# Kernel tuning notes

Hardware: AMD Instinct MI355X
Metric: run time of the kernel (lower is better)

The kernel has to match this reference:

```python
import jax, jax.numpy as jnp
import numpy as np

NUM_EMB = 16384
EMB_DIM = 64
BETA = 0.25  # commitment_cost, legacy=True formulation


def _l2norm(x, axis=-1):
    # matches F.normalize(p=2): x / max(||x||, 1e-12)
    n = jnp.sqrt(jnp.sum(x * x, axis=axis, keepdims=True))
    return x / jnp.maximum(n, 1e-12)


def setup_inputs() -> dict:
    key = jax.random.key(0)
    k_z, k_cb, k_w, k_b = jax.random.split(key, 4)
    z = jax.random.normal(k_z, (16, 1024, EMB_DIM), dtype=jnp.float32)
    # frozen codebook: N(0, d^{-0.5})
    codebook = jax.random.normal(k_cb, (NUM_EMB, EMB_DIM), dtype=jnp.float32) * (EMB_DIM ** -0.5)
    # Linear(d, d) default init: U(-1/sqrt(d), 1/sqrt(d))
    lim = 1.0 / np.sqrt(EMB_DIM)
    proj_w = jax.random.uniform(k_w, (EMB_DIM, EMB_DIM), dtype=jnp.float32, minval=-lim, maxval=lim)
    proj_b = jax.random.uniform(k_b, (EMB_DIM,), dtype=jnp.float32, minval=-lim, maxval=lim)
    scale = jnp.float32(10.0)  # l2_norm_scale
    return {"z": z, "codebook": codebook, "proj_w": proj_w, "proj_b": proj_b, "scale": scale}


def reference(z, codebook, proj_w, proj_b, scale):
    B, T, d = z.shape
    zf = z.reshape(-1, d)                                   # [BT, d]
    quant_codebook = codebook @ proj_w.T + proj_b           # [N, d]
    zn = _l2norm(zf)
    cn = _l2norm(quant_codebook)
    distances = -jnp.einsum('bd,nd->bn', zn, cn) * scale    # [BT, N]
    idx = jnp.argmin(distances, axis=1)                     # [BT]
    quantized = quant_codebook[idx].reshape(z.shape)        # [B, T, d]
    sg = jax.lax.stop_gradient
    commitment_loss = jnp.mean((sg(quantized) - z) ** 2)
    codebook_loss = jnp.mean((quantized - sg(z)) ** 2)
    vq_loss = commitment_loss + BETA * codebook_loss        # legacy=True
    quantized_st = z + sg(quantized - z)                    # straight-through
    return quantized_st, vq_loss, idx.reshape(B, T)
```

## Files before the change

### kernel.cpp

```cpp
#include <hip/hip_runtime.h>
#include <hip/hip_bf16.h>


#define NCODES 16384
#define NTOK   16384
#define DIM    64
#define MARGIN_MFMA 8e-3f

typedef __attribute__((ext_vector_type(8))) short bf16x8;
typedef __attribute__((ext_vector_type(4))) float f32x4;
#define GLOBAL_AS __attribute__((address_space(1)))
#define LDS_AS    __attribute__((address_space(3)))

__device__ float  g_qcb[NCODES * DIM];
__device__ double g_cn64[NCODES * DIM];
__device__ short  g_cnb[NCODES * DIM];
__device__ short  g_znb[NTOK * DIM];
__device__ unsigned g_topu[NTOK];
__device__ int    g_candcnt[NTOK];
__device__ int    g_cand[NTOK * 8];
__device__ int    g_idx[NTOK];
__device__ int    g_ovcnt;
__device__ int    g_ovlist[NTOK];
__device__ float  g_loss;
__device__ int    g_done;

__device__ __forceinline__ float wave_sum64(float v) {
#pragma unroll
  for (int o = 32; o > 0; o >>= 1) v += __shfl_xor(v, o, 64);
  return v;
}
__device__ __forceinline__ double wave_sum64d(double v) {
#pragma unroll
  for (int o = 32; o > 0; o >>= 1) v += __shfl_xor(v, o, 64);
  return v;
}
__device__ __forceinline__ short f2bf(float f) {
  __hip_bfloat16 h = __float2bfloat16(f);
  return *reinterpret_cast<short*>(&h);
}

__global__ __launch_bounds__(256) void k_prep(const float* __restrict__ cb,
                                              const float* __restrict__ pw,
                                              const float* __restrict__ pb,
                                              const float* __restrict__ z) {
  int tid = threadIdx.x;
  if (blockIdx.x < 512) {
    __shared__ float Wt[64 * 65];
    __shared__ float cbs[32 * 65];
    int base = blockIdx.x * 32;
    for (int e = tid; e < 4096; e += 256) {
      int j = e >> 6, k = e & 63;
      Wt[k * 65 + j] = pw[e];
    }
    for (int e = tid; e < 2048; e += 256) {
      int row = e >> 6, k = e & 63;
      cbs[row * 65 + k] = cb[(size_t)(base + row) * 64 + k];
    }
    __syncthreads();
    int w = tid >> 6, j = tid & 63;
    double bj = (double)pb[j];
    for (int rr = 0; rr < 8; ++rr) {
      int nl = w * 8 + rr;
      int n = base + nl;
      double acc = bj;
#pragma unroll
      for (int k = 0; k < 64; ++k)
        acc = fma((double)cbs[nl * 65 + k], (double)Wt[k * 65 + j], acc);
      g_qcb[(size_t)n * 64 + j] = (float)acc;
      double tot = wave_sum64d(acc * acc);
      double cn = acc / fmax(sqrt(tot), 1e-12);
      g_cn64[(size_t)n * 64 + j] = cn;
      g_cnb[(size_t)n * 64 + j] = f2bf((float)cn);
    }
  } else {
    int zb = blockIdx.x - 512;
    int gid = zb * 256 + tid;
    if (gid < NTOK) { g_topu[gid] = 0u; g_candcnt[gid] = 0; }
    if (gid == 0) { g_loss = 0.f; g_ovcnt = 0; g_done = 0; }
    int w = tid >> 6, j = tid & 63;
    int base = zb * 64;
    for (int r = 0; r < 16; ++r) {
      int row = base + w * 16 + r;
      float v = z[(size_t)row * 64 + j];
      float tot = wave_sum64(v * v);
      g_znb[(size_t)row * 64 + j] = f2bf(v / fmaxf(sqrtf(tot), 1e-12f));
    }
  }
}


__global__ __launch_bounds__(256) void k_mfma1() {
  __shared__ __align__(16) short smB[2][8192];
  int tid = threadIdx.x;
  int wave = tid >> 6, lane = tid & 63;
  int quad = lane >> 4, col = lane & 15;
  int tokBlock = blockIdx.x >> 3, split = blockIdx.x & 7;
  int tokBase = tokBlock * 128 + wave * 32;

  const short* za = g_znb + (size_t)(tokBase + col) * 64 + quad * 8;
  bf16x8 A0[2], A1[2];
#pragma unroll
  for (int f = 0; f < 2; ++f) {
    A0[f] = *(const bf16x8*)(za + f * 16 * 64);
    A1[f] = *(const bf16x8*)(za + f * 16 * 64 + 32);
  }
  float m[2][4];
#pragma unroll
  for (int f = 0; f < 2; ++f)
#pragma unroll
    for (int r = 0; r < 4; ++r) m[f][r] = -3.0e38f;

  const char* gsplit = (const char*)(g_cnb + (size_t)split * 2048 * 64);
  int x = col & 7;
  int s0off = ((quad ^ x) << 3);
  int s1off = (((4 | quad) ^ x) << 3);

  int goff[4];
#pragma unroll
  for (int i = 0; i < 4; ++i) {
    int cidx = wave * 256 + i * 64 + lane;
    int row = cidx >> 3, sw = cidx & 7;
    goff[i] = row * 128 + (sw ^ (row & 7)) * 16;
  }

#pragma unroll
  for (int i = 0; i < 4; ++i)
    __builtin_amdgcn_global_load_lds((const GLOBAL_AS void*)(gsplit + goff[i]),
                                     (LDS_AS void*)(&smB[0][wave * 2048 + i * 512]), 16, 0, 0);
  __syncthreads();

  int p = 0;
  for (int s = 0; s < 16; ++s) {
    if (s < 15) {
      const char* gb = gsplit + (size_t)(s + 1) * 16384;
#pragma unroll
      for (int i = 0; i < 4; ++i)
        __builtin_amdgcn_global_load_lds((const GLOBAL_AS void*)(gb + goff[i]),
                                         (LDS_AS void*)(&smB[p ^ 1][wave * 2048 + i * 512]),
                                         16, 0, 0);
    }
    const short* bufp = smB[p];
#pragma unroll
    for (int t = 0; t < 8; ++t) {
      const short* lb = bufp + (t * 16 + col) * 64;
      bf16x8 b0 = *(const bf16x8*)(lb + s0off);
      bf16x8 b1 = *(const bf16x8*)(lb + s1off);
#pragma unroll
      for (int f = 0; f < 2; ++f) {
        f32x4 acc = {0.f, 0.f, 0.f, 0.f};
        acc = __builtin_amdgcn_mfma_f32_16x16x32_bf16(A0[f], b0, acc, 0, 0, 0);
        acc = __builtin_amdgcn_mfma_f32_16x16x32_bf16(A1[f], b1, acc, 0, 0, 0);
#pragma unroll
        for (int r = 0; r < 4; ++r) m[f][r] = fmaxf(m[f][r], acc[r]);
      }
    }
    __syncthreads();
    p ^= 1;
  }

#pragma unroll
  for (int f = 0; f < 2; ++f)
#pragma unroll
    for (int r = 0; r < 4; ++r) {
      float v = m[f][r];
      v = fmaxf(v, __shfl_xor(v, 1, 64));
      v = fmaxf(v, __shfl_xor(v, 2, 64));
      v = fmaxf(v, __shfl_xor(v, 4, 64));
      v = fmaxf(v, __shfl_xor(v, 8, 64));
      if (col == 0) {
        unsigned b = __float_as_uint(v);
        unsigned e = (b & 0x80000000u) ? ~b : (b | 0x80000000u);
        atomicMax(&g_topu[tokBase + f * 16 + quad * 4 + r], e);
      }
    }
}

__global__ __launch_bounds__(256) void k_mfma2() {
  __shared__ __align__(16) short smB[2][8192];
  int tid = threadIdx.x;
  int wave = tid >> 6, lane = tid & 63;
  int quad = lane >> 4, col = lane & 15;
  int tokBlock = blockIdx.x >> 3, split = blockIdx.x & 7;
  int tokBase = tokBlock * 128 + wave * 32;

  const short* za = g_znb + (size_t)(tokBase + col) * 64 + quad * 8;
  bf16x8 A0[2], A1[2];
#pragma unroll
  for (int f = 0; f < 2; ++f) {
    A0[f] = *(const bf16x8*)(za + f * 16 * 64);
    A1[f] = *(const bf16x8*)(za + f * 16 * 64 + 32);
  }
  float th[2][4];
#pragma unroll
  for (int f = 0; f < 2; ++f)
#pragma unroll
    for (int r = 0; r < 4; ++r) {
      unsigned u = g_topu[tokBase + f * 16 + quad * 4 + r];
      unsigned b = (u & 0x80000000u) ? (u & 0x7FFFFFFFu) : ~u;
      th[f][r] = __uint_as_float(b) - MARGIN_MFMA;
    }

  const char* gsplit = (const char*)(g_cnb + (size_t)split * 2048 * 64);
  int x = col & 7;
  int s0off = ((quad ^ x) << 3);
  int s1off = (((4 | quad) ^ x) << 3);

  int goff[4];
#pragma unroll
  for (int i = 0; i < 4; ++i) {
    int cidx = wave * 256 + i * 64 + lane;
    int row = cidx >> 3, sw = cidx & 7;
    goff[i] = row * 128 + (sw ^ (row & 7)) * 16;
  }

#pragma unroll
  for (int i = 0; i < 4; ++i)
    __builtin_amdgcn_global_load_lds((const GLOBAL_AS void*)(gsplit + goff[i]),
                                     (LDS_AS void*)(&smB[0][wave * 2048 + i * 512]), 16, 0, 0);
  __syncthreads();

  int codeB = split * 2048 + col;
  int p = 0;
  for (int s = 0; s < 16; ++s) {
    if (s < 15) {
      const char* gb = gsplit + (size_t)(s + 1) * 16384;
#pragma unroll
      for (int i = 0; i < 4; ++i)
        __builtin_amdgcn_global_load_lds((const GLOBAL_AS void*)(gb + goff[i]),
                                         (LDS_AS void*)(&smB[p ^ 1][wave * 2048 + i * 512]),
                                         16, 0, 0);
    }
    const short* bufp = smB[p];
#pragma unroll
    for (int t = 0; t < 8; ++t) {
      const short* lb = bufp + (t * 16 + col) * 64;
      bf16x8 b0 = *(const bf16x8*)(lb + s0off);
      bf16x8 b1 = *(const bf16x8*)(lb + s1off);
      int code = codeB + s * 128 + t * 16;
#pragma unroll
      for (int f = 0; f < 2; ++f) {
        f32x4 acc = {0.f, 0.f, 0.f, 0.f};
        acc = __builtin_amdgcn_mfma_f32_16x16x32_bf16(A0[f], b0, acc, 0, 0, 0);
        acc = __builtin_amdgcn_mfma_f32_16x16x32_bf16(A1[f], b1, acc, 0, 0, 0);
        float dmax = fmaxf(fmaxf(acc[0] - th[f][0], acc[1] - th[f][1]),
                           fmaxf(acc[2] - th[f][2], acc[3] - th[f][3]));
        if (dmax >= 0.f) {
#pragma unroll
          for (int r = 0; r < 4; ++r) {
            if (acc[r] >= th[f][r]) {
              int tok = tokBase + f * 16 + quad * 4 + r;
              int pos = atomicAdd(&g_candcnt[tok], 1);
              if (pos < 8) g_cand[tok * 8 + pos] = code;
            }
          }
        }
      }
    }
    __syncthreads();
    p ^= 1;
  }
}

__global__ __launch_bounds__(256) void k_exact(const float* __restrict__ z) {
  int tok = blockIdx.x * 256 + threadIdx.x;
  if (tok >= NTOK) return;
  int cnt = g_candcnt[tok];
  if (cnt <= 1) { g_idx[tok] = g_cand[tok * 8]; return; }
  if (cnt > 8) {
    int p = atomicAdd(&g_ovcnt, 1);
    g_ovlist[p] = tok;
    return;
  }
  double zr[64];
#pragma unroll
  for (int k = 0; k < 64; ++k) zr[k] = (double)z[(size_t)tok * 64 + k];
  double best = -1.0e300;
  int bi = 0x7FFFFFFF;
  for (int c = 0; c < cnt; ++c) {
    int code = g_cand[tok * 8 + c];
    const double* cr = g_cn64 + (size_t)code * 64;
    double d = 0.0;
#pragma unroll
    for (int k = 0; k < 64; ++k) d = fma(zr[k], cr[k], d);
    if (d > best || (d == best && code < bi)) { best = d; bi = code; }
  }
  g_idx[tok] = bi;
}

__global__ __launch_bounds__(256) void k_fullscan(const float* __restrict__ z) {
  __shared__ double zn[64];
  __shared__ double rb[256];
  __shared__ int ri[256];
  int tid = threadIdx.x;
  int nov = g_ovcnt;
  for (int f = blockIdx.x; f < nov; f += gridDim.x) {
    int tok = g_ovlist[f];
    if (tid < 64) zn[tid] = (double)z[(size_t)tok * 64 + tid];
    __syncthreads();
    double best = -1.0e300;
    int bi = 0x7FFFFFFF;
    for (int c = tid; c < NCODES; c += 256) {
      const double* cr = g_cn64 + (size_t)c * 64;
      double d0 = 0.0, d1 = 0.0;
#pragma unroll
      for (int k = 0; k < 64; k += 2) {
        d0 = fma(zn[k], cr[k], d0);
        d1 = fma(zn[k + 1], cr[k + 1], d1);
      }
      double d = d0 + d1;
      if (d > best || (d == best && c < bi)) { best = d; bi = c; }
    }
    rb[tid] = best;
    ri[tid] = bi;
    __syncthreads();
    if (tid == 0) {
      double B = rb[0];
      int I = ri[0];
      for (int xx = 1; xx < 256; ++xx)
        if (rb[xx] > B || (rb[xx] == B && ri[xx] < I)) { B = rb[xx]; I = ri[xx]; }
      g_idx[tok] = I;
    }
    __syncthreads();
  }
}

__global__ __launch_bounds__(256) void k_out(const float* __restrict__ z,
                                             float* __restrict__ out0,
                                             float* __restrict__ out1,
                                             float* __restrict__ out2) {
  int tid = threadIdx.x;
  int w = tid >> 6, j = tid & 63;
  int base = blockIdx.x * 64;
  float lsum = 0.f;
  for (int r = 0; r < 16; ++r) {
    int tok = base + w * 16 + r;
    int idx = g_idx[tok];
    float q = g_qcb[(size_t)idx * 64 + j];
    float zv = z[(size_t)tok * 64 + j];
    float d = q - zv;
    out0[(size_t)tok * 64 + j] = zv + d;
    lsum = fmaf(d, d, lsum);
    if (j == 0) out2[tok] = (float)idx;
  }
  float tot = wave_sum64(lsum);
  if (j == 0) atomicAdd(&g_loss, tot);
  __syncthreads();
  if (tid == 0) {
    __threadfence();
    int d = atomicAdd(&g_done, 1);
    if (d == (int)gridDim.x - 1) {
      __threadfence();
      float lv = atomicAdd(&g_loss, 0.0f);
      out1[0] = 1.25f * lv / 1048576.0f;
    }
  }
}

extern "C" void kernel_launch(void* const* d_in, const int* in_sizes, int n_in,
                              void* d_out, int out_size, void* d_ws, size_t ws_size,
                              hipStream_t stream) {
  const float* z = (const float*)d_in[0];
  const float* cb = (const float*)d_in[1];
  const float* pw = (const float*)d_in[2];
  const float* pb = (const float*)d_in[3];

  float* out0 = (float*)d_out;
  float* out1 = out0 + (size_t)NTOK * DIM;
  float* out2 = out1 + 1;

  hipLaunchKernelGGL(k_prep, dim3(768), dim3(256), 0, stream, cb, pw, pb, z);
  hipLaunchKernelGGL(k_mfma1, dim3(1024), dim3(256), 0, stream);
  hipLaunchKernelGGL(k_mfma2, dim3(1024), dim3(256), 0, stream);
  hipLaunchKernelGGL(k_exact, dim3(64), dim3(256), 0, stream, z);
  hipLaunchKernelGGL(k_fullscan, dim3(64), dim3(256), 0, stream, z);
  hipLaunchKernelGGL(k_out, dim3(256), dim3(256), 0, stream, z, out0, out1, out2);
}
```

Before: 205.7 us.

## Use split-bf16 MFMA codebook projection, finer code splits, fuse rescoring into output kernel

The codebook projection now runs on bf16 MFMA with a hi/lo split instead of scalar fp64 loops, and the fp64 normalized codebook buffer is gone. The two MFMA scan kernels split the codes 16 ways instead of 8, which doubles the grid and halves shared memory per block. Candidate capacity rises to 16. Exact rescoring and the full-scan fallback are merged into the output kernel, which recomputes projected codes in fp64 per candidate. This cuts launches and fp64 memory traffic, but the split-bf16 projection may be less precise and the in-kernel fallback scan is very slow if a token overflows.

```diff
diff --git a/kernel.cpp b/kernel.cpp
--- a/kernel.cpp
+++ b/kernel.cpp
@@ -6,6 +6,7 @@
 #define NTOK   16384
 #define DIM    64
 #define MARGIN_MFMA 8e-3f
+#define CAP    16
 
 typedef __attribute__((ext_vector_type(8))) short bf16x8;
 typedef __attribute__((ext_vector_type(4))) float f32x4;
@@ -13,15 +14,11 @@
 #define LDS_AS    __attribute__((address_space(3)))
 
 __device__ float  g_qcb[NCODES * DIM];
-__device__ double g_cn64[NCODES * DIM];
 __device__ short  g_cnb[NCODES * DIM];
 __device__ short  g_znb[NTOK * DIM];
 __device__ unsigned g_topu[NTOK];
 __device__ int    g_candcnt[NTOK];
-__device__ int    g_cand[NTOK * 8];
-__device__ int    g_idx[NTOK];
-__device__ int    g_ovcnt;
-__device__ int    g_ovlist[NTOK];
+__device__ int    g_cand[NTOK * CAP];
 __device__ float  g_loss;
 __device__ int    g_done;
 
@@ -38,6 +35,19 @@
 __device__ __forceinline__ short f2bf(float f) {
   __hip_bfloat16 h = __float2bfloat16(f);
   return *reinterpret_cast<short*>(&h);
+}
+__device__ __forceinline__ float bf2f(short s) {
+  __hip_bfloat16 h = *reinterpret_cast<__hip_bfloat16*>(&s);
+  return __bfloat162float(h);
+}
+__device__ __forceinline__ void split8(const float* v, bf16x8& hi, bf16x8& lo) {
+#pragma unroll
+  for (int i = 0; i < 8; ++i) {
+    float f = v[i];
+    short h = f2bf(f);
+    hi[i] = h;
+    lo[i] = f2bf(f - bf2f(h));
+  }
 }
 
 __global__ __launch_bounds__(256) void k_prep(const float* __restrict__ cb,
@@ -45,40 +55,61 @@
                                               const float* __restrict__ pb,
                                               const float* __restrict__ z) {
   int tid = threadIdx.x;
-  if (blockIdx.x < 512) {
-    __shared__ float Wt[64 * 65];
-    __shared__ float cbs[32 * 65];
-    int base = blockIdx.x * 32;
-    for (int e = tid; e < 4096; e += 256) {
-      int j = e >> 6, k = e & 63;
-      Wt[k * 65 + j] = pw[e];
-    }
-    for (int e = tid; e < 2048; e += 256) {
-      int row = e >> 6, k = e & 63;
-      cbs[row * 65 + k] = cb[(size_t)(base + row) * 64 + k];
-    }
-    __syncthreads();
-    int w = tid >> 6, j = tid & 63;
-    double bj = (double)pb[j];
-    for (int rr = 0; rr < 8; ++rr) {
-      int nl = w * 8 + rr;
-      int n = base + nl;
-      double acc = bj;
-#pragma unroll
-      for (int k = 0; k < 64; ++k)
-        acc = fma((double)cbs[nl * 65 + k], (double)Wt[k * 65 + j], acc);
-      g_qcb[(size_t)n * 64 + j] = (float)acc;
-      double tot = wave_sum64d(acc * acc);
-      double cn = acc / fmax(sqrt(tot), 1e-12);
-      g_cn64[(size_t)n * 64 + j] = cn;
-      g_cnb[(size_t)n * 64 + j] = f2bf((float)cn);
-    }
+  int wave = tid >> 6, lane = tid & 63, quad = lane >> 4, col = lane & 15;
+  if (blockIdx.x < 256) {
+    int rowBase = blockIdx.x * 64 + wave * 16;
+    const float* cr = cb + (size_t)(rowBase + col) * 64 + quad * 8;
+    bf16x8 ah0, al0, ah1, al1;
+    split8(cr, ah0, al0);
+    split8(cr + 32, ah1, al1);
+    float vals[4][4];
+    float nr[4] = {0.f, 0.f, 0.f, 0.f};
+    const f32x4 fz = {0.f, 0.f, 0.f, 0.f};
+#pragma unroll
+    for (int nt = 0; nt < 4; ++nt) {
+      int j = col + 16 * nt;
+      const float* wr = pw + (size_t)j * 64 + quad * 8;
+      bf16x8 bh0, bl0, bh1, bl1;
+      split8(wr, bh0, bl0);
+      split8(wr + 32, bh1, bl1);
+      f32x4 d = __builtin_amdgcn_mfma_f32_16x16x32_bf16(ah0, bh0, fz, 0, 0, 0);
+      d = __builtin_amdgcn_mfma_f32_16x16x32_bf16(ah1, bh1, d, 0, 0, 0);
+      d = __builtin_amdgcn_mfma_f32_16x16x32_bf16(ah0, bl0, d, 0, 0, 0);
+      d = __builtin_amdgcn_mfma_f32_16x16x32_bf16(ah1, bl1, d, 0, 0, 0);
+      d = __builtin_amdgcn_mfma_f32_16x16x32_bf16(al0, bh0, d, 0, 0, 0);
+      d = __builtin_amdgcn_mfma_f32_16x16x32_bf16(al1, bh1, d, 0, 0, 0);
+      float bj = pb[j];
+#pragma unroll
+      for (int r = 0; r < 4; ++r) {
+        float v = d[r] + bj;
+        vals[nt][r] = v;
+        nr[r] = fmaf(v, v, nr[r]);
+      }
+    }
+#pragma unroll
+    for (int r = 0; r < 4; ++r) {
+      float v = nr[r];
+      v += __shfl_xor(v, 1, 64);
+      v += __shfl_xor(v, 2, 64);
+      v += __shfl_xor(v, 4, 64);
+      v += __shfl_xor(v, 8, 64);
+      nr[r] = 1.0f / fmaxf(sqrtf(v), 1e-12f);
+    }
+#pragma unroll
+    for (int nt = 0; nt < 4; ++nt)
+#pragma unroll
+      for (int r = 0; r < 4; ++r) {
+        int row = rowBase + quad * 4 + r;
+        int j = col + 16 * nt;
+        g_qcb[(size_t)row * 64 + j] = vals[nt][r];
+        g_cnb[(size_t)row * 64 + j] = f2bf(vals[nt][r] * nr[r]);
+      }
   } else {
-    int zb = blockIdx.x - 512;
+    int zb = blockIdx.x - 256;
     int gid = zb * 256 + tid;
     if (gid < NTOK) { g_topu[gid] = 0u; g_candcnt[gid] = 0; }
-    if (gid == 0) { g_loss = 0.f; g_ovcnt = 0; g_done = 0; }
-    int w = tid >> 6, j = tid & 63;
+    if (gid == 0) { g_loss = 0.f; g_done = 0; }
+    int w = wave, j = lane;
     int base = zb * 64;
     for (int r = 0; r < 16; ++r) {
       int row = base + w * 16 + r;
@@ -89,13 +120,12 @@
   }
 }
 
-
 __global__ __launch_bounds__(256) void k_mfma1() {
-  __shared__ __align__(16) short smB[2][8192];
+  __shared__ __align__(16) short smB[2][4096];
   int tid = threadIdx.x;
   int wave = tid >> 6, lane = tid & 63;
   int quad = lane >> 4, col = lane & 15;
-  int tokBlock = blockIdx.x >> 3, split = blockIdx.x & 7;
+  int tokBlock = blockIdx.x >> 4, split = blockIdx.x & 15;
   int tokBase = tokBlock * 128 + wave * 32;
 
   const short* za = g_znb + (size_t)(tokBase + col) * 64 + quad * 8;
@@ -111,45 +141,44 @@
 #pragma unroll
     for (int r = 0; r < 4; ++r) m[f][r] = -3.0e38f;
 
-  const char* gsplit = (const char*)(g_cnb + (size_t)split * 2048 * 64);
+  const char* gsplit = (const char*)(g_cnb + (size_t)split * 1024 * 64);
   int x = col & 7;
   int s0off = ((quad ^ x) << 3);
   int s1off = (((4 | quad) ^ x) << 3);
-
-  int goff[4];
-#pragma unroll
-  for (int i = 0; i < 4; ++i) {
-    int cidx = wave * 256 + i * 64 + lane;
+  int goff[2];
+#pragma unroll
+  for (int i = 0; i < 2; ++i) {
+    int cidx = wave * 128 + i * 64 + lane;
     int row = cidx >> 3, sw = cidx & 7;
-    goff[i] = row * 128 + (sw ^ (row & 7)) * 16;
-  }
-
-#pragma unroll
-  for (int i = 0; i < 4; ++i)
+    goff[i] = row * 128 + ((sw ^ (row & 7)) << 4);
+  }
+  const f32x4 fz = {0.f, 0.f, 0.f, 0.f};
+
+#pragma unroll
+  for (int i = 0; i < 2; ++i)
     __builtin_amdgcn_global_load_lds((const GLOBAL_AS void*)(gsplit + goff[i]),
-                                     (LDS_AS void*)(&smB[0][wave * 2048 + i * 512]), 16, 0, 0);
+                                     (LDS_AS void*)(&smB[0][wave * 1024 + i * 512]), 16, 0, 0);
   __syncthreads();
 
   int p = 0;
   for (int s = 0; s < 16; ++s) {
     if (s < 15) {
-      const char* gb = gsplit + (size_t)(s + 1) * 16384;
-#pragma unroll
-      for (int i = 0; i < 4; ++i)
+      const char* gb = gsplit + (size_t)(s + 1) * 8192;
+#pragma unroll
+      for (int i = 0; i < 2; ++i)
         __builtin_amdgcn_global_load_lds((const GLOBAL_AS void*)(gb + goff[i]),
-                                         (LDS_AS void*)(&smB[p ^ 1][wave * 2048 + i * 512]),
+                                         (LDS_AS void*)(&smB[p ^ 1][wave * 1024 + i * 512]),
                                          16, 0, 0);
     }
     const short* bufp = smB[p];
 #pragma unroll
-    for (int t = 0; t < 8; ++t) {
+    for (int t = 0; t < 4; ++t) {
       const short* lb = bufp + (t * 16 + col) * 64;
       bf16x8 b0 = *(const bf16x8*)(lb + s0off);
       bf16x8 b1 = *(const bf16x8*)(lb + s1off);
 #pragma unroll
       for (int f = 0; f < 2; ++f) {
-        f32x4 acc = {0.f, 0.f, 0.f, 0.f};
-        acc = __builtin_amdgcn_mfma_f32_16x16x32_bf16(A0[f], b0, acc, 0, 0, 0);
+        f32x4 acc = __builtin_amdgcn_mfma_f32_16x16x32_bf16(A0[f], b0, fz, 0, 0, 0);
         acc = __builtin_amdgcn_mfma_f32_16x16x32_bf16(A1[f], b1, acc, 0, 0, 0);
 #pragma unroll
         for (int r = 0; r < 4; ++r) m[f][r] = fmaxf(m[f][r], acc[r]);
@@ -177,11 +206,11 @@
 }
 
 __global__ __launch_bounds__(256) void k_mfma2() {
-  __shared__ __align__(16) short smB[2][8192];
+  __shared__ __align__(16) short smB[2][4096];
   int tid = threadIdx.x;
   int wave = tid >> 6, lane = tid & 63;
   int quad = lane >> 4, col = lane & 15;
-  int tokBlock = blockIdx.x >> 3, split = blockIdx.x & 7;
+  int tokBlock = blockIdx.x >> 4, split = blockIdx.x & 15;
   int tokBase = tokBlock * 128 + wave * 32;
 
   const short* za = g_znb + (size_t)(tokBase + col) * 64 + quad * 8;
@@ -201,47 +230,46 @@
       th[f][r] = __uint_as_float(b) - MARGIN_MFMA;
     }
 
-  const char* gsplit = (const char*)(g_cnb + (size_t)split * 2048 * 64);
+  const char* gsplit = (const char*)(g_cnb + (size_t)split * 1024 * 64);
   int x = col & 7;
   int s0off = ((quad ^ x) << 3);
   int s1off = (((4 | quad) ^ x) << 3);
-
-  int goff[4];
-#pragma unroll
-  for (int i = 0; i < 4; ++i) {
-    int cidx = wave * 256 + i * 64 + lane;
+  int goff[2];
+#pragma unroll
+  for (int i = 0; i < 2; ++i) {
+    int cidx = wave * 128 + i * 64 + lane;
     int row = cidx >> 3, sw = cidx & 7;
-    goff[i] = row * 128 + (sw ^ (row & 7)) * 16;
-  }
-
-#pragma unroll
-  for (int i = 0; i < 4; ++i)
+    goff[i] = row * 128 + ((sw ^ (row & 7)) << 4);
+  }
+  const f32x4 fz = {0.f, 0.f, 0.f, 0.f};
+
+#pragma unroll
+  for (int i = 0; i < 2; ++i)
     __builtin_amdgcn_global_load_lds((const GLOBAL_AS void*)(gsplit + goff[i]),
-                                     (LDS_AS void*)(&smB[0][wave * 2048 + i * 512]), 16, 0, 0);
-  __syncthreads();
-
-  int codeB = split * 2048 + col;
+                                     (LDS_AS void*)(&smB[0][wave * 1024 + i * 512]), 16, 0, 0);
+  __syncthreads();
+
+  int codeB = split * 1024 + col;
   int p = 0;
   for (int s = 0; s < 16; ++s) {
     if (s < 15) {
-      const char* gb = gsplit + (size_t)(s + 1) * 16384;
-#pragma unroll
-      for (int i = 0; i < 4; ++i)
+      const char* gb = gsplit + (size_t)(s + 1) * 8192;
+#pragma unroll
+      for (int i = 0; i < 2; ++i)
         __builtin_amdgcn_global_load_lds((const GLOBAL_AS void*)(gb + goff[i]),
-                                         (LDS_AS void*)(&smB[p ^ 1][wave * 2048 + i * 512]),
+                                         (LDS_AS void*)(&smB[p ^ 1][wave * 1024 + i * 512]),
                                          16, 0, 0);
     }
     const short* bufp = smB[p];
 #pragma unroll
-    for (int t = 0; t < 8; ++t) {
+    for (int t = 0; t < 4; ++t) {
       const short* lb = bufp + (t * 16 + col) * 64;
       bf16x8 b0 = *(const bf16x8*)(lb + s0off);
       bf16x8 b1 = *(const bf16x8*)(lb + s1off);
-      int code = codeB + s * 128 + t * 16;
+      int code = codeB + s * 64 + t * 16;
 #pragma unroll
       for (int f = 0; f < 2; ++f) {
-        f32x4 acc = {0.f, 0.f, 0.f, 0.f};
-        acc = __builtin_amdgcn_mfma_f32_16x16x32_bf16(A0[f], b0, acc, 0, 0, 0);
+        f32x4 acc = __builtin_amdgcn_mfma_f32_16x16x32_bf16(A0[f], b0, fz, 0, 0, 0);
         acc = __builtin_amdgcn_mfma_f32_16x16x32_bf16(A1[f], b1, acc, 0, 0, 0);
         float dmax = fmaxf(fmaxf(acc[0] - th[f][0], acc[1] - th[f][1]),
                            fmaxf(acc[2] - th[f][2], acc[3] - th[f][3]));
@@ -251,7 +279,7 @@
             if (acc[r] >= th[f][r]) {
               int tok = tokBase + f * 16 + quad * 4 + r;
               int pos = atomicAdd(&g_candcnt[tok], 1);
-              if (pos < 8) g_cand[tok * 8 + pos] = code;
+              if (pos < CAP) g_cand[tok * CAP + pos] = code;
             }
           }
         }
@@ -262,80 +290,79 @@
   }
 }
 
-__global__ __launch_bounds__(256) void k_exact(const float* __restrict__ z) {
-  int tok = blockIdx.x * 256 + threadIdx.x;
-  if (tok >= NTOK) return;
-  int cnt = g_candcnt[tok];
-  if (cnt <= 1) { g_idx[tok] = g_cand[tok * 8]; return; }
-  if (cnt > 8) {
-    int p = atomicAdd(&g_ovcnt, 1);
-    g_ovlist[p] = tok;
-    return;
-  }
-  double zr[64];
-#pragma unroll
-  for (int k = 0; k < 64; ++k) zr[k] = (double)z[(size_t)tok * 64 + k];
-  double best = -1.0e300;
-  int bi = 0x7FFFFFFF;
-  for (int c = 0; c < cnt; ++c) {
-    int code = g_cand[tok * 8 + c];
-    const double* cr = g_cn64 + (size_t)code * 64;
-    double d = 0.0;
-#pragma unroll
-    for (int k = 0; k < 64; ++k) d = fma(zr[k], cr[k], d);
-    if (d > best || (d == best && code < bi)) { best = d; bi = code; }
-  }
-  g_idx[tok] = bi;
-}
-
-__global__ __launch_bounds__(256) void k_fullscan(const float* __restrict__ z) {
-  __shared__ double zn[64];
-  __shared__ double rb[256];
-  __shared__ int ri[256];
+__global__ __launch_bounds__(256) void k_final(const float* __restrict__ z,
+                                               const float* __restrict__ cb,
+                                               const float* __restrict__ pw,
+                                               const float* __restrict__ pb,
+                                               float* __restrict__ out0,
+                                               float* __restrict__ out1,
+                                               float* __restrict__ out2) {
+  __shared__ double Wl[64 * 65];
+  __shared__ int wl[64];
+  __shared__ int idxs[64];
+  __shared__ int nfl;
   int tid = threadIdx.x;
-  int nov = g_ovcnt;
-  for (int f = blockIdx.x; f < nov; f += gridDim.x) {
-    int tok = g_ovlist[f];
-    if (tid < 64) zn[tid] = (double)z[(size_t)tok * 64 + tid];
-    __syncthreads();
+  int wave = tid >> 6, lane = tid & 63;
+  int base = blockIdx.x * 64;
+
+  for (int e = tid; e < 4096; e += 256) {
+    int j = e >> 6, k = e & 63;
+    Wl[j * 65 + k] = (double)pw[(size_t)j * 64 + k];
+  }
+  if (tid == 0) nfl = 0;
+  __syncthreads();
+  if (tid < 64) {
+    int tok = base + tid;
+    int cnt = g_candcnt[tok];
+    if (cnt <= 1) idxs[tid] = g_cand[tok * CAP];
+    else { int p = atomicAdd(&nfl, 1); wl[p] = tid; }
+  }
+  __syncthreads();
+  int n = nfl;
+  for (int e = wave; e < n; e += 4) {
+    int tl = wl[e];
+    int tok = base + tl;
+    int cnt = g_candcnt[tok];
+    double zj = (double)z[(size_t)tok * 64 + lane];
+    double bj = (double)pb[lane];
     double best = -1.0e300;
     int bi = 0x7FFFFFFF;
-    for (int c = tid; c < NCODES; c += 256) {
-      const double* cr = g_cn64 + (size_t)c * 64;
-      double d0 = 0.0, d1 = 0.0;
-#pragma unroll
-      for (int k = 0; k < 64; k += 2) {
-        d0 = fma(zn[k], cr[k], d0);
-        d1 = fma(zn[k + 1], cr[k + 1], d1);
-      }
-      double d = d0 + d1;
-      if (d > best || (d == best && c < bi)) { best = d; bi = c; }
-    }
-    rb[tid] = best;
-    ri[tid] = bi;
-    __syncthreads();
-    if (tid == 0) {
-      double B = rb[0];
-      int I = ri[0];
-      for (int xx = 1; xx < 256; ++xx)
-        if (rb[xx] > B || (rb[xx] == B && ri[xx] < I)) { B = rb[xx]; I = ri[xx]; }
-      g_idx[tok] = I;
-    }
-    __syncthreads();
-  }
-}
-
-__global__ __launch_bounds__(256) void k_out(const float* __restrict__ z,
-                                             float* __restrict__ out0,
-                                             float* __restrict__ out1,
-                                             float* __restrict__ out2) {
-  int tid = threadIdx.x;
-  int w = tid >> 6, j = tid & 63;
-  int base = blockIdx.x * 64;
+    int lim = (cnt <= CAP) ? cnt : 0;
+    for (int c = 0; c < lim; ++c) {
+      int code = g_cand[tok * CAP + c];
+      float cbv = cb[(size_t)code * 64 + lane];
+      double acc = bj;
+#pragma unroll
+      for (int k = 0; k < 64; ++k)
+        acc = fma((double)__shfl(cbv, k, 64), Wl[lane * 65 + k], acc);
+      double s = wave_sum64d(zj * acc);
+      double n2 = wave_sum64d(acc * acc);
+      double key = s / fmax(sqrt(n2), 1e-12);
+      if (key > best || (key == best && code < bi)) { best = key; bi = code; }
+    }
+    if (cnt > CAP) {
+      for (int code = 0; code < NCODES; ++code) {
+        float cbv = cb[(size_t)code * 64 + lane];
+        double acc = bj;
+#pragma unroll
+        for (int k = 0; k < 64; ++k)
+          acc = fma((double)__shfl(cbv, k, 64), Wl[lane * 65 + k], acc);
+        double s = wave_sum64d(zj * acc);
+        double n2 = wave_sum64d(acc * acc);
+        double key = s / fmax(sqrt(n2), 1e-12);
+        if (key > best || (key == best && code < bi)) { best = key; bi = code; }
+      }
+    }
+    if (lane == 0) idxs[tl] = bi;
+  }
+  __syncthreads();
+
+  int w = wave, j = lane;
   float lsum = 0.f;
   for (int r = 0; r < 16; ++r) {
-    int tok = base + w * 16 + r;
-    int idx = g_idx[tok];
+    int tl = w * 16 + r;
+    int tok = base + tl;
+    int idx = idxs[tl];
     float q = g_qcb[(size_t)idx * 64 + j];
     float zv = z[(size_t)tok * 64 + j];
     float d = q - zv;
@@ -369,10 +396,8 @@
   float* out1 = out0 + (size_t)NTOK * DIM;
   float* out2 = out1 + 1;
 
-  hipLaunchKernelGGL(k_prep, dim3(768), dim3(256), 0, stream, cb, pw, pb, z);
-  hipLaunchKernelGGL(k_mfma1, dim3(1024), dim3(256), 0, stream);
-  hipLaunchKernelGGL(k_mfma2, dim3(1024), dim3(256), 0, stream);
-  hipLaunchKernelGGL(k_exact, dim3(64), dim3(256), 0, stream, z);
-  hipLaunchKernelGGL(k_fullscan, dim3(64), dim3(256), 0, stream, z);
-  hipLaunchKernelGGL(k_out, dim3(256), dim3(256), 0, stream, z, out0, out1, out2);
-}
+  hipLaunchKernelGGL(k_prep, dim3(512), dim3(256), 0, stream, cb, pw, pb, z);
+  hipLaunchKernelGGL(k_mfma1, dim3(2048), dim3(256), 0, stream);
+  hipLaunchKernelGGL(k_mfma2, dim3(2048), dim3(256), 0, stream);
+  hipLaunchKernelGGL(k_final, dim3(256), dim3(256), 0, stream, z, cb, pw, pb, out0, out1, out2);
+}
```

After: 242.0 us. 17.6% more time.
